# Kernel optimization log

Hardware: AMD Instinct MI355X
Metric: run time of the kernel (lower is better)

The kernel has to match this reference:

```python
import jax, jax.numpy as jnp
import numpy as np

N_NODES = 100000
N_EDGES = 1600000
IN_F, HID_F, OUT_F = 128, 128, 64


def setup_inputs() -> dict:
    key = jax.random.key(0)
    ks = jax.random.split(key, 8)
    x = jax.random.normal(ks[0], (N_NODES, IN_F), dtype=jnp.float32)
    edge_index = jax.random.randint(ks[1], (2, N_EDGES), 0, N_NODES, dtype=jnp.int64)
    w1 = jax.random.normal(ks[2], (IN_F, HID_F), dtype=jnp.float32) * 0.05
    b1 = jax.random.normal(ks[3], (HID_F,), dtype=jnp.float32) * 0.05
    c1 = jax.random.normal(ks[4], (IN_F, HID_F, 3), dtype=jnp.float32) * 0.01
    w2 = jax.random.normal(ks[5], (HID_F, OUT_F), dtype=jnp.float32) * 0.05
    b2 = jax.random.normal(ks[6], (OUT_F,), dtype=jnp.float32) * 0.05
    c2 = jax.random.normal(ks[7], (IN_F, OUT_F, 3), dtype=jnp.float32) * 0.01
    return {"x": x, "edge_index": edge_index, "w1": w1, "b1": b1, "c1": c1,
            "w2": w2, "b2": b2, "c2": c2}


def _minimal_kan(x, w, b, c):
    # linear term: (N, out)
    lin = x @ w + b
    # polynomial basis (x, x^2, x^3): (N, in, 3)
    basis = jnp.stack([x, x * x, x * x * x], axis=-1)
    # fused contraction over (in, 3); same math as the (N,in,out,3) broadcast-sum
    kan_out = jnp.einsum('nib,iob->no', basis, c)
    return lin + 0.1 * kan_out


def _aggregate(h, source, target, num_nodes):
    # mean over incoming messages, degree clamped at 1
    deg = jax.ops.segment_sum(jnp.ones(source.shape[0], dtype=h.dtype), target,
                              num_segments=num_nodes)
    deg = jnp.maximum(deg, 1.0)
    out = jax.ops.segment_sum(h[source], target, num_segments=num_nodes)
    return out / deg[:, None]


def reference(x, edge_index, w1, b1, c1, w2, b2, c2):
    source, target = edge_index[0], edge_index[1]
    n = x.shape[0]
    h = _minimal_kan(x, w1, b1, c1)
    h = jax.nn.relu(h)
    h = _aggregate(h, source, target, n)
    h = _minimal_kan(h, w2, b2, c2)
    h = _aggregate(h, source, target, n)
    return jax.nn.log_softmax(h, axis=-1)
```

## Files before the change

kernel.cpp:

```cpp
#include <hip/hip_runtime.h>
#include <hip/hip_bf16.h>
#include <math.h>

#define N_NODES 100000
#define N_EDGES 1600000
#define IN_F 128
#define HID_F 128
#define OUT_F 64
#define K_TOT 384
#define BST 392

#define BK_BITS 9
#define BK_SIZE 512
#define NBUCK ((N_NODES + BK_SIZE - 1) / BK_SIZE)
#define EPB 4096
#define NBLK_SORT ((N_EDGES + EPB - 1) / EPB)
#define BCAP 10240
#define PCAP (BCAP + 7 * BK_SIZE)
#define PK_SRC_MASK 0x7fffffu
#define PAD8(d) (((d) + 7) & ~7)

typedef __attribute__((ext_vector_type(8))) short s8v;
typedef __attribute__((ext_vector_type(4))) short s4v;
typedef __attribute__((ext_vector_type(4))) float f4v;
typedef __attribute__((ext_vector_type(2))) float f2v;

__device__ __forceinline__ short f2bf(float f) {
    __hip_bfloat16 h = __float2bfloat16(f);
    return __builtin_bit_cast(short, h);
}

__global__ __launch_bounds__(256) void fold_weights_bf16(
    const float* __restrict__ w1, const float* __restrict__ c1,
    const float* __restrict__ w2, const float* __restrict__ c2,
    short* __restrict__ Wb1, short* __restrict__ Wb2,
    unsigned* __restrict__ h1d, unsigned* __restrict__ h2d,
    int* __restrict__ bcur)
{
    if (blockIdx.x == 0) {
        if (threadIdx.x < 32) h1d[(size_t)N_NODES * 32 + threadIdx.x] = 0;
        if (threadIdx.x < 16) h2d[(size_t)N_NODES * 16 + threadIdx.x] = 0;
        if (threadIdx.x < NBUCK) bcur[threadIdx.x] = threadIdx.x * BCAP;
    }
    int idx = blockIdx.x * 256 + threadIdx.x;
    if (idx < K_TOT * HID_F) {
        int k = idx >> 7, n = idx & 127;
        int p = k >> 7, f = k & 127;
        int si = f * HID_F + n;
        float v = (p == 0) ? (w1[si] + 0.1f * c1[si * 3])
                           : 0.1f * c1[si * 3 + p];
        Wb1[(((k >> 3) * HID_F) + n) * 8 + (k & 7)] = f2bf(v);
    } else {
        idx -= K_TOT * HID_F;
        if (idx < K_TOT * OUT_F) {
            int k = idx >> 6, n = idx & 63;
            int p = k >> 7, f = k & 127;
            int si = f * OUT_F + n;
            float v = (p == 0) ? (w2[si] + 0.1f * c2[si * 3])
                               : 0.1f * c2[si * 3 + p];
            Wb2[(((k >> 3) * OUT_F) + n) * 8 + (k & 7)] = f2bf(v);
        }
    }
}

__global__ __launch_bounds__(256) void bucket_scatter(
    const int* __restrict__ src, const int* __restrict__ tgt,
    int* __restrict__ bcur, unsigned* __restrict__ spk)
{
    __shared__ int h[NBUCK];
    __shared__ int base[NBUCK];
    __shared__ int tg[EPB];
    int tid = threadIdx.x;
    for (int i = tid; i < NBUCK; i += 256) h[i] = 0;
    __syncthreads();
    int e0 = blockIdx.x * EPB;
    int n = min(EPB, N_EDGES - e0);
    for (int i = tid; i < n; i += 256) {
        int t = tgt[e0 + i];
        tg[i] = t;
        atomicAdd(&h[t >> BK_BITS], 1);
    }
    __syncthreads();
    for (int i = tid; i < NBUCK; i += 256) {
        int c = h[i];
        base[i] = c ? atomicAdd(&bcur[i], c) : 0;
        h[i] = 0;
    }
    __syncthreads();
    for (int i = tid; i < n; i += 256) {
        int t = tg[i];
        int b = t >> BK_BITS;
        int pos = base[b] + atomicAdd(&h[b], 1);
        spk[pos] = ((unsigned)(t - (b << BK_BITS)) << 23) | (unsigned)src[e0 + i];
    }
}

__global__ __launch_bounds__(256) void csr_build(
    const int* __restrict__ bcur, const unsigned* __restrict__ spk,
    int* __restrict__ deg, int* __restrict__ prow, int* __restrict__ csr_pad)
{
    __shared__ int d[BK_SIZE];
    __shared__ int pst[BK_SIZE];
    __shared__ int s[256];
    int tid = threadIdx.x;
    int b = blockIdx.x;
    d[tid] = 0; d[tid + 256] = 0;
    __syncthreads();
    int e0 = b * BCAP, e1 = bcur[b];
    for (int i = e0 + tid; i < e1; i += 256)
        atomicAdd(&d[spk[i] >> 23], 1);
    __syncthreads();
    int nbase = b << BK_BITS;
    int a0 = d[2 * tid], a1c = d[2 * tid + 1];
    int n0 = nbase + 2 * tid, n1 = n0 + 1;
    if (n0 < N_NODES) deg[n0] = a0;
    if (n1 < N_NODES) deg[n1] = a1c;
    int pc0 = (n0 < N_NODES) ? PAD8(a0) : 0;
    int pc1 = (n1 < N_NODES) ? PAD8(a1c) : 0;
    int tsum = pc0 + pc1;
    s[tid] = tsum;
    __syncthreads();
    for (int o = 1; o < 256; o <<= 1) {
        int t = (tid >= o) ? s[tid - o] : 0;
        __syncthreads();
        s[tid] += t;
        __syncthreads();
    }
    int excl = s[tid] - tsum;
    int base = b * PCAP + excl;
    if (n0 < N_NODES) prow[n0] = base;
    if (n1 < N_NODES) prow[n1] = base + pc0;
    __syncthreads();
    d[2 * tid] = base;         pst[2 * tid]     = base + pc0;
    d[2 * tid + 1] = base + pc0; pst[2 * tid + 1] = base + pc0 + pc1;
    __syncthreads();
    for (int i = e0 + tid; i < e1; i += 256) {
        unsigned pk = spk[i];
        int pos = atomicAdd(&d[pk >> 23], 1);
        csr_pad[pos] = (int)(pk & PK_SRC_MASK);
    }
    __syncthreads();
    for (int i = tid; i < BK_SIZE; i += 256) {
        int nd = nbase + i;
        if (nd < N_NODES) {
            int kend = pst[i];
            for (int k = d[i]; k < kend; ++k) csr_pad[k] = N_NODES;
        }
    }
}

__global__ __launch_bounds__(256) void kan1_mfma(
    const float* __restrict__ x, const short* __restrict__ Wb,
    const float* __restrict__ bias, unsigned* __restrict__ h1d)
{
    __shared__ short sb[64 * BST];
    const int tid  = threadIdx.x;
    const int lane = tid & 63;
    const int wave = tid >> 6;
    const int node0 = blockIdx.x * 64;
    const int q = lane >> 4, r = lane & 15;

#pragma unroll
    for (int it = 0; it < 8; ++it) {
        int idx = tid + 256 * it;
        int m = idx >> 5, c4 = (idx & 31) * 4;
        int gm = min(node0 + m, N_NODES - 1);
        float4 v = *(const float4*)(x + (size_t)gm * IN_F + c4);
        float vv[4] = {v.x, v.y, v.z, v.w};
        s4v p0, p1, p2;
#pragma unroll
        for (int t = 0; t < 4; ++t) {
            float e = vv[t], e2 = e * e, e3 = e2 * e;
            p0[t] = f2bf(e); p1[t] = f2bf(e2); p2[t] = f2bf(e3);
        }
        short* row = sb + m * BST + c4;
        *(s4v*)(row)       = p0;
        *(s4v*)(row + 128) = p1;
        *(s4v*)(row + 256) = p2;
    }
    __syncthreads();

    const int wm = (wave & 1) * 32;
    const int wn = (wave >> 1) * 64;

    f4v acc[2][4];
#pragma unroll
    for (int i = 0; i < 2; ++i)
#pragma unroll
        for (int j = 0; j < 4; ++j)
            acc[i][j] = (f4v){0.f, 0.f, 0.f, 0.f};

    float bj[4];
#pragma unroll
    for (int j = 0; j < 4; ++j) bj[j] = bias[wn + j * 16 + r];

#pragma unroll
    for (int kb = 0; kb < 12; ++kb) {
        const int col = kb * 32 + q * 8;
        s8v afrag[2];
#pragma unroll
        for (int i = 0; i < 2; ++i)
            afrag[i] = *(const s8v*)(sb + (wm + i * 16 + r) * BST + col);
#pragma unroll
        for (int j = 0; j < 4; ++j) {
            const s8v b = *(const s8v*)(Wb + (((kb * 4 + q) * HID_F) + wn + j * 16 + r) * 8);
            acc[0][j] = __builtin_amdgcn_mfma_f32_16x16x32_bf16(afrag[0], b, acc[0][j], 0, 0, 0);
            acc[1][j] = __builtin_amdgcn_mfma_f32_16x16x32_bf16(afrag[1], b, acc[1][j], 0, 0, 0);
        }
    }

    const int dci = ((wn >> 6) << 4) + r;
#pragma unroll
    for (int i = 0; i < 2; ++i)
#pragma unroll
        for (int e = 0; e < 4; ++e) {
            int grow = node0 + wm + i * 16 + q * 4 + e;
            if (grow < N_NODES) {
                float v0 = fmaxf(acc[i][0][e] + bj[0], 0.f);
                float v1 = fmaxf(acc[i][1][e] + bj[1], 0.f);
                float v2 = fmaxf(acc[i][2][e] + bj[2], 0.f);
                float v3 = fmaxf(acc[i][3][e] + bj[3], 0.f);
                int pk = __builtin_amdgcn_cvt_pk_fp8_f32(v0, v1, 0, false);
                pk = __builtin_amdgcn_cvt_pk_fp8_f32(v2, v3, pk, true);
                h1d[(size_t)grow * 32 + dci] = (unsigned)pk;
            }
        }
}

__global__ __launch_bounds__(256) void gather128(
    const unsigned* __restrict__ h1d, const int* __restrict__ prow,
    const int* __restrict__ deg, const int* __restrict__ csr_pad,
    unsigned* __restrict__ a1d)
{
    const int lane  = threadIdx.x & 63;
    const int wave  = threadIdx.x >> 6;
    const int hl    = lane & 31;
    const int half  = lane >> 5;
    const int hbase = half << 5;
    const int node  = blockIdx.x * 8 + wave * 2 + half;

    int p0 = prow[node];
    int cnt = PAD8(deg[node]);
    int p1 = p0 + cnt;
    int cmax = max(cnt, __shfl_xor(cnt, 32));

    float acc[4][4];
#pragma unroll
    for (int t = 0; t < 4; ++t)
#pragma unroll
        for (int b = 0; b < 4; ++b) acc[t][b] = 0.f;

    for (int base = 0; base < cmax; base += 32) {
        int idx = max(min(p0 + base + hl, p1 - 1), 0);
        int sreg = csr_pad[idx];
        int lim = min(32, cmax - base);
        for (int j = 0; j < lim; j += 4) {
            if (base + j < cnt) {
                unsigned u[4];
#pragma unroll
                for (int t = 0; t < 4; ++t) {
                    int sj = __shfl(sreg, hbase + j + t);
                    u[t] = h1d[(size_t)sj * 32 + hl];
                }
#pragma unroll
                for (int t = 0; t < 4; ++t) {
                    f2v lo = __builtin_amdgcn_cvt_pk_f32_fp8(u[t], false);
                    f2v hi = __builtin_amdgcn_cvt_pk_f32_fp8(u[t], true);
                    acc[t][0] += lo.x; acc[t][1] += lo.y;
                    acc[t][2] += hi.x; acc[t][3] += hi.y;
                }
            }
        }
    }

    float s0 = (acc[0][0] + acc[1][0]) + (acc[2][0] + acc[3][0]);
    float s1 = (acc[0][1] + acc[1][1]) + (acc[2][1] + acc[3][1]);
    float s2 = (acc[0][2] + acc[1][2]) + (acc[2][2] + acc[3][2]);
    float s3 = (acc[0][3] + acc[1][3]) + (acc[2][3] + acc[3][3]);
    int pk = __builtin_amdgcn_cvt_pk_fp8_f32(s0, s1, 0, false);
    pk = __builtin_amdgcn_cvt_pk_fp8_f32(s2, s3, pk, true);
    a1d[(size_t)node * 32 + hl] = (unsigned)pk;
}

__global__ __launch_bounds__(256) void kan2_mfma(
    const unsigned* __restrict__ a1d, const int* __restrict__ deg,
    const short* __restrict__ Wb, const float* __restrict__ bias,
    unsigned short* __restrict__ h2s)
{
    __shared__ short sb[64 * BST];
    const int tid  = threadIdx.x;
    const int lane = tid & 63;
    const int wave = tid >> 6;
    const int node0 = blockIdx.x * 64;
    const int q = lane >> 4, r = lane & 15;

#pragma unroll
    for (int gi = 0; gi < 2; ++gi) {
        int g = tid + 256 * gi;
        int m = g >> 3, cg = (g & 7) * 4;
        int gm = min(node0 + m, N_NODES - 1);
        float di = 1.0f / fmaxf((float)deg[gm], 1.0f);
        uint4 u4 = *(const uint4*)(a1d + (size_t)gm * 32 + cg);
        unsigned uw[4] = {u4.x, u4.y, u4.z, u4.w};
        float xv[4][4];
#pragma unroll
        for (int j = 0; j < 4; ++j) {
            f2v lo = __builtin_amdgcn_cvt_pk_f32_fp8(uw[j], false);
            f2v hi = __builtin_amdgcn_cvt_pk_f32_fp8(uw[j], true);
            xv[j][0] = lo.x * di; xv[j][1] = lo.y * di;
            xv[j][2] = hi.x * di; xv[j][3] = hi.y * di;
        }
        int fb = ((cg >> 4) << 6) + (cg & 15);
#pragma unroll
        for (int b = 0; b < 4; ++b) {
            s4v p0, p1, p2;
#pragma unroll
            for (int j = 0; j < 4; ++j) {
                float e = xv[j][b], e2 = e * e, e3 = e2 * e;
                p0[j] = f2bf(e); p1[j] = f2bf(e2); p2[j] = f2bf(e3);
            }
            short* row = sb + m * BST + fb + 16 * b;
            *(s4v*)(row)       = p0;
            *(s4v*)(row + 128) = p1;
            *(s4v*)(row + 256) = p2;
        }
    }
    __syncthreads();

    const int wm = (wave & 1) * 32;
    const int wn = (wave >> 1) * 32;

    f4v acc[2][2];
#pragma unroll
    for (int i = 0; i < 2; ++i)
#pragma unroll
        for (int j = 0; j < 2; ++j)
            acc[i][j] = (f4v){0.f, 0.f, 0.f, 0.f};

    float bj[2];
#pragma unroll
    for (int j = 0; j < 2; ++j) bj[j] = bias[wn + j * 16 + r];

#pragma unroll
    for (int kb = 0; kb < 12; ++kb) {
        const int col = kb * 32 + q * 8;
        s8v afrag[2];
#pragma unroll
        for (int i = 0; i < 2; ++i)
            afrag[i] = *(const s8v*)(sb + (wm + i * 16 + r) * BST + col);
#pragma unroll
        for (int j = 0; j < 2; ++j) {
            const s8v b = *(const s8v*)(Wb + (((kb * 4 + q) * OUT_F) + wn + j * 16 + r) * 8);
            acc[0][j] = __builtin_amdgcn_mfma_f32_16x16x32_bf16(afrag[0], b, acc[0][j], 0, 0, 0);
            acc[1][j] = __builtin_amdgcn_mfma_f32_16x16x32_bf16(afrag[1], b, acc[1][j], 0, 0, 0);
        }
    }

    const int sslot = (wn >> 1) + r;
#pragma unroll
    for (int i = 0; i < 2; ++i)
#pragma unroll
        for (int e = 0; e < 4; ++e) {
            int grow = node0 + wm + i * 16 + q * 4 + e;
            if (grow < N_NODES) {
                float vlo = acc[i][0][e] + bj[0];
                float vhi = acc[i][1][e] + bj[1];
                int pk = __builtin_amdgcn_cvt_pk_fp8_f32(vlo, vhi, 0, false);
                h2s[(size_t)grow * 32 + sslot] = (unsigned short)(pk & 0xffff);
            }
        }
}

__global__ __launch_bounds__(256) void gather64_lsm(
    const unsigned short* __restrict__ h2s, const int* __restrict__ deg,
    const int* __restrict__ prow, const int* __restrict__ csr_pad,
    float* __restrict__ out)
{
    const int lane = threadIdx.x & 63;
    const int wave = threadIdx.x >> 6;
    const int hl   = lane & 31;
    const int half = lane >> 5;
    const int node = blockIdx.x * 8 + wave * 2 + half;

    int p0 = prow[node];
    int degr = deg[node];
    int cnt = PAD8(degr);
    int p1 = p0 + cnt;
    int cmax = max(cnt, __shfl_xor(cnt, 32));

    float alo[8], ahi[8];
#pragma unroll
    for (int t = 0; t < 8; ++t) { alo[t] = 0.f; ahi[t] = 0.f; }

    for (int base = 0; base < cmax; base += 32) {
        int idx = max(min(p0 + base + hl, p1 - 1), 0);
        int sreg = csr_pad[idx];
        int lim = min(32, cmax - base);
        for (int j = 0; j < lim; j += 8) {
            if (base + j < cnt) {
                int u[8];
#pragma unroll
                for (int t = 0; t < 8; ++t) {
                    int sj = __shfl(sreg, (half << 5) + j + t);
                    u[t] = (int)h2s[(size_t)sj * 32 + hl];
                }
#pragma unroll
                for (int t = 0; t < 8; ++t) {
                    alo[t] += __builtin_amdgcn_cvt_f32_fp8(u[t], 0);
                    ahi[t] += __builtin_amdgcn_cvt_f32_fp8(u[t], 1);
                }
            }
        }
    }
    float slo = ((alo[0] + alo[1]) + (alo[2] + alo[3])) + ((alo[4] + alo[5]) + (alo[6] + alo[7]));
    float shi = ((ahi[0] + ahi[1]) + (ahi[2] + ahi[3])) + ((ahi[4] + ahi[5]) + (ahi[6] + ahi[7]));

    float di = 1.0f / fmaxf((float)degr, 1.0f);
    float vlo = slo * di, vhi = shi * di;

    float m = fmaxf(vlo, vhi);
#pragma unroll
    for (int off = 16; off >= 1; off >>= 1)
        m = fmaxf(m, __shfl_xor(m, off));
    float e = expf(vlo - m) + expf(vhi - m);
#pragma unroll
    for (int off = 16; off >= 1; off >>= 1)
        e += __shfl_xor(e, off);
    float ls = logf(e);

    const int f_lo = ((hl >> 4) << 5) + (hl & 15);
    out[(size_t)node * OUT_F + f_lo]      = vlo - m - ls;
    out[(size_t)node * OUT_F + f_lo + 16] = vhi - m - ls;
}

extern "C" void kernel_launch(void* const* d_in, const int* in_sizes, int n_in,
                              void* d_out, int out_size, void* d_ws, size_t ws_size,
                              hipStream_t stream)
{
    const float* x  = (const float*)d_in[0];
    const int*   ei = (const int*)d_in[1];
    const float* w1 = (const float*)d_in[2];
    const float* b1 = (const float*)d_in[3];
    const float* c1 = (const float*)d_in[4];
    const float* w2 = (const float*)d_in[5];
    const float* b2 = (const float*)d_in[6];
    const float* c2 = (const float*)d_in[7];
    float* out = (float*)d_out;

    const int* src = ei;
    const int* tgt = ei + N_EDGES;

    char* ws = (char*)d_ws;
    size_t off = 0;
    auto carve = [&](size_t bytes) -> void* {
        void* p = ws + off;
        off = (off + bytes + 255) & ~(size_t)255;
        return p;
    };
    short*    Wb1       = (short*)carve((size_t)K_TOT * HID_F * 2);
    short*    Wb2       = (short*)carve((size_t)K_TOT * OUT_F * 2);
    int*      deg       = (int*)carve((size_t)N_NODES * 4);
    int*      prow      = (int*)carve((size_t)N_NODES * 4);
    int*      bcur      = (int*)carve((size_t)NBUCK * 4);
    unsigned* spk       = (unsigned*)carve((size_t)NBUCK * BCAP * 4);
    int*      csr_pad   = (int*)carve((size_t)NBUCK * PCAP * 4);
    unsigned* h1d       = (unsigned*)carve(((size_t)N_NODES + 1) * 128);
    unsigned* a1d       = (unsigned*)carve((size_t)N_NODES * 128);
    unsigned short* h2s = (unsigned short*)carve(((size_t)N_NODES + 1) * 64);

    const int grid_mm = (N_NODES + 63) / 64;

    fold_weights_bf16<<<(K_TOT * HID_F + K_TOT * OUT_F + 255) / 256, 256, 0, stream>>>(
        w1, c1, w2, c2, Wb1, Wb2, h1d, (unsigned*)h2s, bcur);

    bucket_scatter<<<NBLK_SORT, 256, 0, stream>>>(src, tgt, bcur, spk);
    csr_build<<<NBUCK, 256, 0, stream>>>(bcur, spk, deg, prow, csr_pad);

    kan1_mfma<<<grid_mm, 256, 0, stream>>>(x, Wb1, b1, h1d);

    gather128<<<(N_NODES + 7) / 8, 256, 0, stream>>>(h1d, prow, deg, csr_pad, a1d);

    kan2_mfma<<<grid_mm, 256, 0, stream>>>(a1d, deg, Wb2, b2, h2s);

    gather64_lsm<<<(N_NODES + 7) / 8, 256, 0, stream>>>(
        h2s, deg, prow, csr_pad, out);
}
```

Measured before the change: 249.9 us.

## Fuse bucket scatter with KAN1 and fuse first gather into KAN2

Merges the edge bucket scatter and the first KAN MFMA layer into one launch, with blocks split by blockIdx so the independent work runs concurrently. The first-layer neighbor gather is folded into the second KAN kernel: each block gathers its 64 nodes' mean features directly into shared memory, dropping the a1d intermediate buffer and its fp8 round trip. This removes two launches and a global write and read, but gather_kan2 now has only 64-node blocks (fewer, heavier blocks), which may reduce latency hiding for the irregular gather.

```diff
diff --git a/kernel.cpp b/kernel.cpp
--- a/kernel.cpp
+++ b/kernel.cpp
@@ -63,101 +63,48 @@
     }
 }
 
-__global__ __launch_bounds__(256) void bucket_scatter(
+__global__ __launch_bounds__(256) void scatter_kan1(
     const int* __restrict__ src, const int* __restrict__ tgt,
-    int* __restrict__ bcur, unsigned* __restrict__ spk)
-{
-    __shared__ int h[NBUCK];
-    __shared__ int base[NBUCK];
-    __shared__ int tg[EPB];
-    int tid = threadIdx.x;
-    for (int i = tid; i < NBUCK; i += 256) h[i] = 0;
-    __syncthreads();
-    int e0 = blockIdx.x * EPB;
-    int n = min(EPB, N_EDGES - e0);
-    for (int i = tid; i < n; i += 256) {
-        int t = tgt[e0 + i];
-        tg[i] = t;
-        atomicAdd(&h[t >> BK_BITS], 1);
-    }
-    __syncthreads();
-    for (int i = tid; i < NBUCK; i += 256) {
-        int c = h[i];
-        base[i] = c ? atomicAdd(&bcur[i], c) : 0;
-        h[i] = 0;
-    }
-    __syncthreads();
-    for (int i = tid; i < n; i += 256) {
-        int t = tg[i];
-        int b = t >> BK_BITS;
-        int pos = base[b] + atomicAdd(&h[b], 1);
-        spk[pos] = ((unsigned)(t - (b << BK_BITS)) << 23) | (unsigned)src[e0 + i];
-    }
-}
-
-__global__ __launch_bounds__(256) void csr_build(
-    const int* __restrict__ bcur, const unsigned* __restrict__ spk,
-    int* __restrict__ deg, int* __restrict__ prow, int* __restrict__ csr_pad)
-{
-    __shared__ int d[BK_SIZE];
-    __shared__ int pst[BK_SIZE];
-    __shared__ int s[256];
-    int tid = threadIdx.x;
-    int b = blockIdx.x;
-    d[tid] = 0; d[tid + 256] = 0;
-    __syncthreads();
-    int e0 = b * BCAP, e1 = bcur[b];
-    for (int i = e0 + tid; i < e1; i += 256)
-        atomicAdd(&d[spk[i] >> 23], 1);
-    __syncthreads();
-    int nbase = b << BK_BITS;
-    int a0 = d[2 * tid], a1c = d[2 * tid + 1];
-    int n0 = nbase + 2 * tid, n1 = n0 + 1;
-    if (n0 < N_NODES) deg[n0] = a0;
-    if (n1 < N_NODES) deg[n1] = a1c;
-    int pc0 = (n0 < N_NODES) ? PAD8(a0) : 0;
-    int pc1 = (n1 < N_NODES) ? PAD8(a1c) : 0;
-    int tsum = pc0 + pc1;
-    s[tid] = tsum;
-    __syncthreads();
-    for (int o = 1; o < 256; o <<= 1) {
-        int t = (tid >= o) ? s[tid - o] : 0;
-        __syncthreads();
-        s[tid] += t;
-        __syncthreads();
-    }
-    int excl = s[tid] - tsum;
-    int base = b * PCAP + excl;
-    if (n0 < N_NODES) prow[n0] = base;
-    if (n1 < N_NODES) prow[n1] = base + pc0;
-    __syncthreads();
-    d[2 * tid] = base;         pst[2 * tid]     = base + pc0;
-    d[2 * tid + 1] = base + pc0; pst[2 * tid + 1] = base + pc0 + pc1;
-    __syncthreads();
-    for (int i = e0 + tid; i < e1; i += 256) {
-        unsigned pk = spk[i];
-        int pos = atomicAdd(&d[pk >> 23], 1);
-        csr_pad[pos] = (int)(pk & PK_SRC_MASK);
-    }
-    __syncthreads();
-    for (int i = tid; i < BK_SIZE; i += 256) {
-        int nd = nbase + i;
-        if (nd < N_NODES) {
-            int kend = pst[i];
-            for (int k = d[i]; k < kend; ++k) csr_pad[k] = N_NODES;
-        }
-    }
-}
-
-__global__ __launch_bounds__(256) void kan1_mfma(
+    int* __restrict__ bcur, unsigned* __restrict__ spk,
     const float* __restrict__ x, const short* __restrict__ Wb,
     const float* __restrict__ bias, unsigned* __restrict__ h1d)
 {
-    __shared__ short sb[64 * BST];
-    const int tid  = threadIdx.x;
+    __shared__ __align__(16) char smem[64 * BST * 2];
+    const int tid = threadIdx.x;
+
+    if (blockIdx.x < NBLK_SORT) {
+        int* h    = (int*)smem;
+        int* base = h + NBUCK;
+        int* tg   = base + NBUCK;
+        for (int i = tid; i < NBUCK; i += 256) h[i] = 0;
+        __syncthreads();
+        int e0 = blockIdx.x * EPB;
+        int n = min(EPB, N_EDGES - e0);
+        for (int i = tid; i < n; i += 256) {
+            int t = tgt[e0 + i];
+            tg[i] = t;
+            atomicAdd(&h[t >> BK_BITS], 1);
+        }
+        __syncthreads();
+        for (int i = tid; i < NBUCK; i += 256) {
+            int c = h[i];
+            base[i] = c ? atomicAdd(&bcur[i], c) : 0;
+            h[i] = 0;
+        }
+        __syncthreads();
+        for (int i = tid; i < n; i += 256) {
+            int t = tg[i];
+            int b = t >> BK_BITS;
+            int pos = base[b] + atomicAdd(&h[b], 1);
+            spk[pos] = ((unsigned)(t - (b << BK_BITS)) << 23) | (unsigned)src[e0 + i];
+        }
+        return;
+    }
+
+    short* sb = (short*)smem;
     const int lane = tid & 63;
     const int wave = tid >> 6;
-    const int node0 = blockIdx.x * 64;
+    const int node0 = (blockIdx.x - NBLK_SORT) * 64;
     const int q = lane >> 4, r = lane & 15;
 
 #pragma unroll
@@ -227,63 +174,63 @@
         }
 }
 
-__global__ __launch_bounds__(256) void gather128(
+__global__ __launch_bounds__(256) void csr_build(
+    const int* __restrict__ bcur, const unsigned* __restrict__ spk,
+    int* __restrict__ deg, int* __restrict__ prow, int* __restrict__ csr_pad)
+{
+    __shared__ int d[BK_SIZE];
+    __shared__ int pst[BK_SIZE];
+    __shared__ int s[256];
+    int tid = threadIdx.x;
+    int b = blockIdx.x;
+    d[tid] = 0; d[tid + 256] = 0;
+    __syncthreads();
+    int e0 = b * BCAP, e1 = bcur[b];
+    for (int i = e0 + tid; i < e1; i += 256)
+        atomicAdd(&d[spk[i] >> 23], 1);
+    __syncthreads();
+    int nbase = b << BK_BITS;
+    int a0 = d[2 * tid], a1c = d[2 * tid + 1];
+    int n0 = nbase + 2 * tid, n1 = n0 + 1;
+    if (n0 < N_NODES) deg[n0] = a0;
+    if (n1 < N_NODES) deg[n1] = a1c;
+    int pc0 = (n0 < N_NODES) ? PAD8(a0) : 0;
+    int pc1 = (n1 < N_NODES) ? PAD8(a1c) : 0;
+    int tsum = pc0 + pc1;
+    s[tid] = tsum;
+    __syncthreads();
+    for (int o = 1; o < 256; o <<= 1) {
+        int t = (tid >= o) ? s[tid - o] : 0;
+        __syncthreads();
+        s[tid] += t;
+        __syncthreads();
+    }
+    int excl = s[tid] - tsum;
+    int base = b * PCAP + excl;
+    if (n0 < N_NODES) prow[n0] = base;
+    if (n1 < N_NODES) prow[n1] = base + pc0;
+    __syncthreads();
+    d[2 * tid] = base;         pst[2 * tid]     = base + pc0;
+    d[2 * tid + 1] = base + pc0; pst[2 * tid + 1] = base + pc0 + pc1;
+    __syncthreads();
+    for (int i = e0 + tid; i < e1; i += 256) {
+        unsigned pk = spk[i];
+        int pos = atomicAdd(&d[pk >> 23], 1);
+        csr_pad[pos] = (int)(pk & PK_SRC_MASK);
+    }
+    __syncthreads();
+    for (int i = tid; i < BK_SIZE; i += 256) {
+        int nd = nbase + i;
+        if (nd < N_NODES) {
+            int kend = pst[i];
+            for (int k = d[i]; k < kend; ++k) csr_pad[k] = N_NODES;
+        }
+    }
+}
+
+__global__ __launch_bounds__(256) void gather_kan2(
     const unsigned* __restrict__ h1d, const int* __restrict__ prow,
     const int* __restrict__ deg, const int* __restrict__ csr_pad,
-    unsigned* __restrict__ a1d)
-{
-    const int lane  = threadIdx.x & 63;
-    const int wave  = threadIdx.x >> 6;
-    const int hl    = lane & 31;
-    const int half  = lane >> 5;
-    const int hbase = half << 5;
-    const int node  = blockIdx.x * 8 + wave * 2 + half;
-
-    int p0 = prow[node];
-    int cnt = PAD8(deg[node]);
-    int p1 = p0 + cnt;
-    int cmax = max(cnt, __shfl_xor(cnt, 32));
-
-    float acc[4][4];
-#pragma unroll
-    for (int t = 0; t < 4; ++t)
-#pragma unroll
-        for (int b = 0; b < 4; ++b) acc[t][b] = 0.f;
-
-    for (int base = 0; base < cmax; base += 32) {
-        int idx = max(min(p0 + base + hl, p1 - 1), 0);
-        int sreg = csr_pad[idx];
-        int lim = min(32, cmax - base);
-        for (int j = 0; j < lim; j += 4) {
-            if (base + j < cnt) {
-                unsigned u[4];
-#pragma unroll
-                for (int t = 0; t < 4; ++t) {
-                    int sj = __shfl(sreg, hbase + j + t);
-                    u[t] = h1d[(size_t)sj * 32 + hl];
-                }
-#pragma unroll
-                for (int t = 0; t < 4; ++t) {
-                    f2v lo = __builtin_amdgcn_cvt_pk_f32_fp8(u[t], false);
-                    f2v hi = __builtin_amdgcn_cvt_pk_f32_fp8(u[t], true);
-                    acc[t][0] += lo.x; acc[t][1] += lo.y;
-                    acc[t][2] += hi.x; acc[t][3] += hi.y;
-                }
-            }
-        }
-    }
-
-    float s0 = (acc[0][0] + acc[1][0]) + (acc[2][0] + acc[3][0]);
-    float s1 = (acc[0][1] + acc[1][1]) + (acc[2][1] + acc[3][1]);
-    float s2 = (acc[0][2] + acc[1][2]) + (acc[2][2] + acc[3][2]);
-    float s3 = (acc[0][3] + acc[1][3]) + (acc[2][3] + acc[3][3]);
-    int pk = __builtin_amdgcn_cvt_pk_fp8_f32(s0, s1, 0, false);
-    pk = __builtin_amdgcn_cvt_pk_fp8_f32(s2, s3, pk, true);
-    a1d[(size_t)node * 32 + hl] = (unsigned)pk;
-}
-
-__global__ __launch_bounds__(256) void kan2_mfma(
-    const unsigned* __restrict__ a1d, const int* __restrict__ deg,
     const short* __restrict__ Wb, const float* __restrict__ bias,
     unsigned short* __restrict__ h2s)
 {
@@ -291,42 +238,68 @@
     const int tid  = threadIdx.x;
     const int lane = tid & 63;
     const int wave = tid >> 6;
+    const int hl   = lane & 31;
+    const int half = lane >> 5;
+    const int hbase = half << 5;
     const int node0 = blockIdx.x * 64;
+    const int hw = wave * 2 + half;
+    const int fpos = ((hl >> 4) << 6) + (hl & 15);
+
+    for (int s = 0; s < 8; ++s) {
+        const int m = hw * 8 + s;
+        const int node = node0 + m;
+        const bool valid = node < N_NODES;
+        int p0  = valid ? prow[node] : 0;
+        int dg  = valid ? deg[node] : 0;
+        int cnt = PAD8(dg);
+        int p1  = p0 + cnt;
+        int cmax = max(cnt, __shfl_xor(cnt, 32));
+
+        float a[2][4];
+#pragma unroll
+        for (int t = 0; t < 2; ++t)
+#pragma unroll
+            for (int b = 0; b < 4; ++b) a[t][b] = 0.f;
+
+        for (int base = 0; base < cmax; base += 32) {
+            int idx = max(min(p0 + base + hl, p1 - 1), 0);
+            int sreg = csr_pad[idx];
+            int lim = min(32, cmax - base);
+            for (int j = 0; j < lim; j += 8) {
+                if (base + j < cnt) {
+                    unsigned u[8];
+#pragma unroll
+                    for (int t = 0; t < 8; ++t) {
+                        int sj = __shfl(sreg, hbase + j + t);
+                        u[t] = h1d[(size_t)sj * 32 + hl];
+                    }
+#pragma unroll
+                    for (int t = 0; t < 8; ++t) {
+                        f2v lo = __builtin_amdgcn_cvt_pk_f32_fp8(u[t], false);
+                        f2v hi = __builtin_amdgcn_cvt_pk_f32_fp8(u[t], true);
+                        a[t & 1][0] += lo.x; a[t & 1][1] += lo.y;
+                        a[t & 1][2] += hi.x; a[t & 1][3] += hi.y;
+                    }
+                }
+            }
+        }
+        float di = 1.0f / fmaxf((float)dg, 1.0f);
+        float sv[4];
+#pragma unroll
+        for (int b = 0; b < 4; ++b) sv[b] = (a[0][b] + a[1][b]) * di;
+
+        short* row = sb + m * BST + fpos;
+#pragma unroll
+        for (int b = 0; b < 4; ++b) {
+            float e = sv[b], e2 = e * e, e3 = e2 * e;
+            row[16 * b]       = f2bf(e);
+            row[16 * b + 128] = f2bf(e2);
+            row[16 * b + 256] = f2bf(e3);
+        }
+    }
+    __syncthreads();
+
     const int q = lane >> 4, r = lane & 15;
-
-#pragma unroll
-    for (int gi = 0; gi < 2; ++gi) {
-        int g = tid + 256 * gi;
-        int m = g >> 3, cg = (g & 7) * 4;
-        int gm = min(node0 + m, N_NODES - 1);
-        float di = 1.0f / fmaxf((float)deg[gm], 1.0f);
-        uint4 u4 = *(const uint4*)(a1d + (size_t)gm * 32 + cg);
-        unsigned uw[4] = {u4.x, u4.y, u4.z, u4.w};
-        float xv[4][4];
-#pragma unroll
-        for (int j = 0; j < 4; ++j) {
-            f2v lo = __builtin_amdgcn_cvt_pk_f32_fp8(uw[j], false);
-            f2v hi = __builtin_amdgcn_cvt_pk_f32_fp8(uw[j], true);
-            xv[j][0] = lo.x * di; xv[j][1] = lo.y * di;
-            xv[j][2] = hi.x * di; xv[j][3] = hi.y * di;
-        }
-        int fb = ((cg >> 4) << 6) + (cg & 15);
-#pragma unroll
-        for (int b = 0; b < 4; ++b) {
-            s4v p0, p1, p2;
-#pragma unroll
-            for (int j = 0; j < 4; ++j) {
-                float e = xv[j][b], e2 = e * e, e3 = e2 * e;
-                p0[j] = f2bf(e); p1[j] = f2bf(e2); p2[j] = f2bf(e3);
-            }
-            short* row = sb + m * BST + fb + 16 * b;
-            *(s4v*)(row)       = p0;
-            *(s4v*)(row + 128) = p1;
-            *(s4v*)(row + 256) = p2;
-        }
-    }
-    __syncthreads();
-
     const int wm = (wave & 1) * 32;
     const int wn = (wave >> 1) * 32;
 
@@ -465,7 +438,6 @@
     unsigned* spk       = (unsigned*)carve((size_t)NBUCK * BCAP * 4);
     int*      csr_pad   = (int*)carve((size_t)NBUCK * PCAP * 4);
     unsigned* h1d       = (unsigned*)carve(((size_t)N_NODES + 1) * 128);
-    unsigned* a1d       = (unsigned*)carve((size_t)N_NODES * 128);
     unsigned short* h2s = (unsigned short*)carve(((size_t)N_NODES + 1) * 64);
 
     const int grid_mm = (N_NODES + 63) / 64;
@@ -473,14 +445,13 @@
     fold_weights_bf16<<<(K_TOT * HID_F + K_TOT * OUT_F + 255) / 256, 256, 0, stream>>>(
         w1, c1, w2, c2, Wb1, Wb2, h1d, (unsigned*)h2s, bcur);
 
-    bucket_scatter<<<NBLK_SORT, 256, 0, stream>>>(src, tgt, bcur, spk);
+    scatter_kan1<<<NBLK_SORT + grid_mm, 256, 0, stream>>>(
+        src, tgt, bcur, spk, x, Wb1, b1, h1d);
+
     csr_build<<<NBUCK, 256, 0, stream>>>(bcur, spk, deg, prow, csr_pad);
 
-    kan1_mfma<<<grid_mm, 256, 0, stream>>>(x, Wb1, b1, h1d);
-
-    gather128<<<(N_NODES + 7) / 8, 256, 0, stream>>>(h1d, prow, deg, csr_pad, a1d);
-
-    kan2_mfma<<<grid_mm, 256, 0, stream>>>(a1d, deg, Wb2, b2, h2s);
+    gather_kan2<<<grid_mm, 256, 0, stream>>>(
+        h1d, prow, deg, csr_pad, Wb2, b2, h2s);
 
     gather64_lsm<<<(N_NODES + 7) / 8, 256, 0, stream>>>(
         h2s, deg, prow, csr_pad, out);
```

New measurement: 258.9 us. 1.04x slower.

## Fuse bucket scatter with KAN1 GEMM in one launch; widen csr_build to 512 threads

Applied to the files above, without the earlier changes.

Merges the edge bucket-scatter kernel and the first KAN MFMA kernel into one launch. Blocks are split by blockIdx: the first blocks do the scatter and the rest do the GEMM, so both independent phases run concurrently and share one shared-memory allocation. csr_build now uses 512 threads, one per node in a bucket, which simplifies the prefix scan and the padding loop. The fused kernel's shared-memory footprint is the larger of the two uses, which can reduce occupancy for the scatter blocks, and the longer scan adds a barrier step.

```diff
diff --git a/kernel.cpp b/kernel.cpp
--- a/kernel.cpp
+++ b/kernel.cpp
@@ -63,101 +63,48 @@
     }
 }
 
-__global__ __launch_bounds__(256) void bucket_scatter(
+__global__ __launch_bounds__(256) void scatter_kan1(
     const int* __restrict__ src, const int* __restrict__ tgt,
-    int* __restrict__ bcur, unsigned* __restrict__ spk)
-{
-    __shared__ int h[NBUCK];
-    __shared__ int base[NBUCK];
-    __shared__ int tg[EPB];
-    int tid = threadIdx.x;
-    for (int i = tid; i < NBUCK; i += 256) h[i] = 0;
-    __syncthreads();
-    int e0 = blockIdx.x * EPB;
-    int n = min(EPB, N_EDGES - e0);
-    for (int i = tid; i < n; i += 256) {
-        int t = tgt[e0 + i];
-        tg[i] = t;
-        atomicAdd(&h[t >> BK_BITS], 1);
-    }
-    __syncthreads();
-    for (int i = tid; i < NBUCK; i += 256) {
-        int c = h[i];
-        base[i] = c ? atomicAdd(&bcur[i], c) : 0;
-        h[i] = 0;
-    }
-    __syncthreads();
-    for (int i = tid; i < n; i += 256) {
-        int t = tg[i];
-        int b = t >> BK_BITS;
-        int pos = base[b] + atomicAdd(&h[b], 1);
-        spk[pos] = ((unsigned)(t - (b << BK_BITS)) << 23) | (unsigned)src[e0 + i];
-    }
-}
-
-__global__ __launch_bounds__(256) void csr_build(
-    const int* __restrict__ bcur, const unsigned* __restrict__ spk,
-    int* __restrict__ deg, int* __restrict__ prow, int* __restrict__ csr_pad)
-{
-    __shared__ int d[BK_SIZE];
-    __shared__ int pst[BK_SIZE];
-    __shared__ int s[256];
-    int tid = threadIdx.x;
-    int b = blockIdx.x;
-    d[tid] = 0; d[tid + 256] = 0;
-    __syncthreads();
-    int e0 = b * BCAP, e1 = bcur[b];
-    for (int i = e0 + tid; i < e1; i += 256)
-        atomicAdd(&d[spk[i] >> 23], 1);
-    __syncthreads();
-    int nbase = b << BK_BITS;
-    int a0 = d[2 * tid], a1c = d[2 * tid + 1];
-    int n0 = nbase + 2 * tid, n1 = n0 + 1;
-    if (n0 < N_NODES) deg[n0] = a0;
-    if (n1 < N_NODES) deg[n1] = a1c;
-    int pc0 = (n0 < N_NODES) ? PAD8(a0) : 0;
-    int pc1 = (n1 < N_NODES) ? PAD8(a1c) : 0;
-    int tsum = pc0 + pc1;
-    s[tid] = tsum;
-    __syncthreads();
-    for (int o = 1; o < 256; o <<= 1) {
-        int t = (tid >= o) ? s[tid - o] : 0;
-        __syncthreads();
-        s[tid] += t;
-        __syncthreads();
-    }
-    int excl = s[tid] - tsum;
-    int base = b * PCAP + excl;
-    if (n0 < N_NODES) prow[n0] = base;
-    if (n1 < N_NODES) prow[n1] = base + pc0;
-    __syncthreads();
-    d[2 * tid] = base;         pst[2 * tid]     = base + pc0;
-    d[2 * tid + 1] = base + pc0; pst[2 * tid + 1] = base + pc0 + pc1;
-    __syncthreads();
-    for (int i = e0 + tid; i < e1; i += 256) {
-        unsigned pk = spk[i];
-        int pos = atomicAdd(&d[pk >> 23], 1);
-        csr_pad[pos] = (int)(pk & PK_SRC_MASK);
-    }
-    __syncthreads();
-    for (int i = tid; i < BK_SIZE; i += 256) {
-        int nd = nbase + i;
-        if (nd < N_NODES) {
-            int kend = pst[i];
-            for (int k = d[i]; k < kend; ++k) csr_pad[k] = N_NODES;
-        }
-    }
-}
-
-__global__ __launch_bounds__(256) void kan1_mfma(
+    int* __restrict__ bcur, unsigned* __restrict__ spk,
     const float* __restrict__ x, const short* __restrict__ Wb,
     const float* __restrict__ bias, unsigned* __restrict__ h1d)
 {
-    __shared__ short sb[64 * BST];
-    const int tid  = threadIdx.x;
+    __shared__ __align__(16) char smem[64 * BST * 2];
+    const int tid = threadIdx.x;
+
+    if (blockIdx.x < NBLK_SORT) {
+        int* h    = (int*)smem;
+        int* base = h + NBUCK;
+        int* tg   = base + NBUCK;
+        for (int i = tid; i < NBUCK; i += 256) h[i] = 0;
+        __syncthreads();
+        int e0 = blockIdx.x * EPB;
+        int n = min(EPB, N_EDGES - e0);
+        for (int i = tid; i < n; i += 256) {
+            int t = tgt[e0 + i];
+            tg[i] = t;
+            atomicAdd(&h[t >> BK_BITS], 1);
+        }
+        __syncthreads();
+        for (int i = tid; i < NBUCK; i += 256) {
+            int c = h[i];
+            base[i] = c ? atomicAdd(&bcur[i], c) : 0;
+            h[i] = 0;
+        }
+        __syncthreads();
+        for (int i = tid; i < n; i += 256) {
+            int t = tg[i];
+            int b = t >> BK_BITS;
+            int pos = base[b] + atomicAdd(&h[b], 1);
+            spk[pos] = ((unsigned)(t - (b << BK_BITS)) << 23) | (unsigned)src[e0 + i];
+        }
+        return;
+    }
+
+    short* sb = (short*)smem;
     const int lane = tid & 63;
     const int wave = tid >> 6;
-    const int node0 = blockIdx.x * 64;
+    const int node0 = (blockIdx.x - NBLK_SORT) * 64;
     const int q = lane >> 4, r = lane & 15;
 
 #pragma unroll
@@ -225,6 +172,53 @@
                 h1d[(size_t)grow * 32 + dci] = (unsigned)pk;
             }
         }
+}
+
+__global__ __launch_bounds__(512) void csr_build(
+    const int* __restrict__ bcur, const unsigned* __restrict__ spk,
+    int* __restrict__ deg, int* __restrict__ prow, int* __restrict__ csr_pad)
+{
+    __shared__ int d[BK_SIZE];
+    __shared__ int pst[BK_SIZE];
+    __shared__ int s[BK_SIZE];
+    int tid = threadIdx.x;
+    int b = blockIdx.x;
+    d[tid] = 0;
+    __syncthreads();
+    int e0 = b * BCAP, e1 = bcur[b];
+    for (int i = e0 + tid; i < e1; i += 512)
+        atomicAdd(&d[spk[i] >> 23], 1);
+    __syncthreads();
+    int nbase = b << BK_BITS;
+    int node = nbase + tid;
+    int a = d[tid];
+    if (node < N_NODES) deg[node] = a;
+    int pc = (node < N_NODES) ? PAD8(a) : 0;
+    s[tid] = pc;
+    __syncthreads();
+    for (int o = 1; o < 512; o <<= 1) {
+        int t = (tid >= o) ? s[tid - o] : 0;
+        __syncthreads();
+        s[tid] += t;
+        __syncthreads();
+    }
+    int excl = s[tid] - pc;
+    int base = b * PCAP + excl;
+    if (node < N_NODES) prow[node] = base;
+    __syncthreads();
+    d[tid] = base;
+    pst[tid] = base + pc;
+    __syncthreads();
+    for (int i = e0 + tid; i < e1; i += 512) {
+        unsigned pk = spk[i];
+        int pos = atomicAdd(&d[pk >> 23], 1);
+        csr_pad[pos] = (int)(pk & PK_SRC_MASK);
+    }
+    __syncthreads();
+    {
+        int kend = pst[tid];
+        for (int k = d[tid]; k < kend; ++k) csr_pad[k] = N_NODES;
+    }
 }
 
 __global__ __launch_bounds__(256) void gather128(
@@ -473,10 +467,10 @@
     fold_weights_bf16<<<(K_TOT * HID_F + K_TOT * OUT_F + 255) / 256, 256, 0, stream>>>(
         w1, c1, w2, c2, Wb1, Wb2, h1d, (unsigned*)h2s, bcur);
 
-    bucket_scatter<<<NBLK_SORT, 256, 0, stream>>>(src, tgt, bcur, spk);
-    csr_build<<<NBUCK, 256, 0, stream>>>(bcur, spk, deg, prow, csr_pad);
-
-    kan1_mfma<<<grid_mm, 256, 0, stream>>>(x, Wb1, b1, h1d);
+    scatter_kan1<<<NBLK_SORT + grid_mm, 256, 0, stream>>>(
+        src, tgt, bcur, spk, x, Wb1, b1, h1d);
+
+    csr_build<<<NBUCK, 512, 0, stream>>>(bcur, spk, deg, prow, csr_pad);
 
     gather128<<<(N_NODES + 7) / 8, 256, 0, stream>>>(h1d, prow, deg, csr_pad, a1d);
 
```

Measured after the change: 231.2 us. 1.08x faster.
